# Optimization experiments

Hardware: AMD Instinct MI355X
Metric: run time of the kernel (lower is better)

The kernel has to match this reference:

```python
import jax, jax.numpy as jnp
import numpy as np

DIM_E, DIM_M, DIM_C = 1024, 64, 128
B, N = 4, 4096


def setup_inputs() -> dict:
    key = jax.random.key(0)
    ks = jax.random.split(key, 10)
    s = 1.0 / np.sqrt(DIM_E + DIM_C)
    return {
        "e": jax.random.normal(ks[0], (B, N, DIM_E), jnp.float32),
        "m": jax.random.normal(ks[1], (B, N, DIM_M), jnp.float32),
        "c": jax.random.normal(ks[2], (B, N, DIM_C), jnp.float32),
        "l": jax.random.uniform(ks[3], (B, N), jnp.float32),
        "Wq": jax.random.uniform(ks[4], (DIM_E + DIM_C, DIM_E), jnp.float32, -s, s),
        "bq": jax.random.uniform(ks[5], (DIM_E,), jnp.float32, -s, s),
        "Wk": jax.random.uniform(ks[6], (DIM_E + DIM_C, DIM_E), jnp.float32, -s, s),
        "bk": jax.random.uniform(ks[7], (DIM_E,), jnp.float32, -s, s),
        "Wv": jax.random.uniform(ks[8], (DIM_E + DIM_C, DIM_E), jnp.float32, -s, s),
        "bv": jax.random.uniform(ks[9], (DIM_E,), jnp.float32, -s, s),
    }


def reference(e, m, c, l, Wq, bq, Wk, bk, Wv, bv):
    x = jnp.concatenate([e, c], axis=-1)                       # [B,N,De+Dc]
    q = jnp.einsum('bnd,df->bnf', x, Wq) + bq                  # [B,N,De]
    k = jnp.einsum('bnd,df->bnf', x, Wk) + bk
    v = jnp.einsum('bnd,df->bnf', x, Wv) + bv
    scale = 1.0 / jnp.sqrt(jnp.asarray(q.shape[-1], q.dtype))
    attn_scores = jnp.einsum('bqd,bkd->bqk', q, k) * scale     # [B,N,N]
    membrane_mask = jnp.einsum('bqm,bkm->bqk', m, m)           # [B,N,N]
    lifespan_mask = l[:, :, None] * l[:, None, :]              # [B,N,N]
    adaptive_scores = attn_scores * membrane_mask * lifespan_mask
    attn_weights = jax.nn.softmax(adaptive_scores, axis=-1)
    h_tilde = jnp.einsum('bqk,bkd->bqd', attn_weights, v)      # [B,N,De]
    e_new = e + h_tilde
    return (e_new, h_tilde)
```

## Files before the change

### kernel.cpp

```cpp
#include <hip/hip_runtime.h>
#include <hip/hip_bf16.h>

#define DE 1024
#define DM 64
#define DC 128
#define DX 1152
#define NB 4
#define NN 4096
#define NT 16384

typedef _Float16 f16;
typedef _Float16 f16x4 __attribute__((ext_vector_type(4)));
typedef _Float16 f16x8 __attribute__((ext_vector_type(8)));
typedef float f32x4 __attribute__((ext_vector_type(4)));

__device__ __forceinline__ void g2l16(const void* g, void* l) {
  __builtin_amdgcn_global_load_lds(
      (const __attribute__((address_space(1))) unsigned int*)(unsigned long long)g,
      (__attribute__((address_space(3))) unsigned int*)(unsigned int)(unsigned long long)l,
      16, 0, 0);
}

__global__ void build_x_kernel(const float* __restrict__ e, const float* __restrict__ c,
                               f16* __restrict__ Xb) {
  const int total = NT * DX / 4;
  for (int i = blockIdx.x * blockDim.x + threadIdx.x; i < total; i += gridDim.x * blockDim.x) {
    int idx = i * 4;
    int r = idx / DX, col = idx - r * DX;
    float4 v;
    if (col < DE) v = *(const float4*)(e + (long)r * DE + col);
    else          v = *(const float4*)(c + (long)r * DC + (col - DE));
    f16x4 o = { (f16)v.x, (f16)v.y, (f16)v.z, (f16)v.w };
    *(f16x4*)(Xb + (long)idx) = o;
  }
}

__global__ void conv_f16_kernel(const float* __restrict__ in, f16* __restrict__ out, int total4) {
  for (int i = blockIdx.x * blockDim.x + threadIdx.x; i < total4; i += gridDim.x * blockDim.x) {
    float4 v = *(const float4*)(in + (long)i * 4);
    f16x4 o = { (f16)v.x, (f16)v.y, (f16)v.z, (f16)v.w };
    *(f16x4*)(out + (long)i * 4) = o;
  }
}

__global__ void transpose_w_kernel(const float* __restrict__ in, f16* __restrict__ out) {
  __shared__ float tile[32][33];
  int c0 = blockIdx.x * 32, r0 = blockIdx.y * 32;
  int x = threadIdx.x, y = threadIdx.y;
#pragma unroll
  for (int i = 0; i < 4; ++i)
    tile[y + 8 * i][x] = in[(long)(r0 + y + 8 * i) * DE + (c0 + x)];
  __syncthreads();
#pragma unroll
  for (int i = 0; i < 4; ++i)
    out[(long)(c0 + y + 8 * i) * DX + (r0 + x)] = (f16)tile[x][y + 8 * i];
}

__device__ __forceinline__ void mm_loop(const f16* __restrict__ A, const f16* __restrict__ B,
                                        int lda, int ldb, int K,
                                        f16* lA, f16* lB, f32x4 (&acc)[4][4]) {
  const int t = threadIdx.x;
  const int lane = t & 63;
  const int wid = t >> 6;
  const int wr = (wid >> 1) * 64, wc = (wid & 1) * 64;
  const int fr = lane & 15, fq = lane >> 4;
  for (int k0 = 0; k0 < K; k0 += 32) {
    __syncthreads();
#pragma unroll
    for (int it = 0; it < 2; ++it) {
      int byteoff = it * 4096 + t * 16;
      int row = byteoff >> 6;
      int ke = (byteoff & 63) >> 1;
      g2l16(A + (long)row * lda + k0 + ke, lA + (byteoff >> 1));
      g2l16(B + (long)row * ldb + k0 + ke, lB + (byteoff >> 1));
    }
    __syncthreads();
    f16x8 af[4], bfr[4];
#pragma unroll
    for (int i = 0; i < 4; ++i) {
      af[i]  = *(const f16x8*)(lA + (wr + i * 16 + fr) * 32 + fq * 8);
      bfr[i] = *(const f16x8*)(lB + (wc + i * 16 + fr) * 32 + fq * 8);
    }
#pragma unroll
    for (int m = 0; m < 4; ++m)
#pragma unroll
      for (int n = 0; n < 4; ++n)
        acc[m][n] = __builtin_amdgcn_mfma_f32_16x16x32_f16(af[m], bfr[n], acc[m][n], 0, 0, 0);
  }
}

__global__ __launch_bounds__(256) void mask_kernel(
    const f16* __restrict__ mb, const float* __restrict__ l, f16* __restrict__ Pm) {
  __shared__ __attribute__((aligned(16))) f16 lA[128 * 32], lB[128 * 32];
  f32x4 acc[4][4];
#pragma unroll
  for (int m = 0; m < 4; ++m)
#pragma unroll
    for (int n = 0; n < 4; ++n) acc[m][n] = (f32x4){0.f, 0.f, 0.f, 0.f};
  const int b = blockIdx.z;
  const int row0 = blockIdx.x * 128, col0 = blockIdx.y * 128;
  mm_loop(mb + (long)(b * NN + row0) * DM, mb + (long)(b * NN + col0) * DM,
          DM, DM, DM, lA, lB, acc);
  const int lane = threadIdx.x & 63, wid = threadIdx.x >> 6;
  const int wr = (wid >> 1) * 64, wc = (wid & 1) * 64;
  const int fr = lane & 15, fq = lane >> 4;
  const float* lb = l + (long)b * NN;
  f16* out = Pm + (long)b * NN * NN;
#pragma unroll
  for (int n = 0; n < 4; ++n) {
    int col = col0 + wc + n * 16 + fr;
    float lc = lb[col] * 0.03125f;
#pragma unroll
    for (int m = 0; m < 4; ++m)
#pragma unroll
      for (int r = 0; r < 4; ++r) {
        int row = row0 + wr + m * 16 + fq * 4 + r;
        out[(long)row * NN + col] = (f16)(acc[m][n][r] * lc * lb[row]);
      }
  }
}

__device__ __forceinline__ void gemm4_core(
    const f16* __restrict__ A, long lda,
    const f16* __restrict__ B, long ldb,
    int NTt, char* ldsb, f32x4 (&acc)[4][4]) {
  const int tid = threadIdx.x;
  const int lane = tid & 63, wid = tid >> 6;
  const int wr = wid >> 1, wc = wid & 1;
  const int fr = lane & 15, fq = lane >> 4;
  const int cb0 = ((fq) ^ (fr & 7)) << 4;
  const int cb1 = ((4 | fq) ^ (fr & 7)) << 4;

  auto stage = [&](const f16* __restrict__ S, long ld, int kt, char* base) {
#pragma unroll
    for (int it = 0; it < 4; ++it) {
      int off = it * 4096 + tid * 16;
      int sw = off ^ (((off >> 7) & 7) << 4);
      int row = sw >> 7;
      int colf = ((sw >> 4) & 7) << 3;
      g2l16(S + (long)row * ld + kt * 64 + colf, base + off);
    }
  };

  stage(A, lda, 0, ldsb);
  stage(B, ldb, 0, ldsb + 16384);
  __syncthreads();

  for (int tt = 0; tt < NTt; ++tt) {
    const int par = tt & 1;
    const char* cur = ldsb + par * 32768;
    char* nxt = ldsb + (par ^ 1) * 32768;
    if (tt + 1 < NTt) {
      stage(A, lda, tt + 1, nxt);
      stage(B, ldb, tt + 1, nxt + 16384);
    }
    __builtin_amdgcn_sched_barrier(0);
    f16x8 a[4][2], b[4][2];
#pragma unroll
    for (int i = 0; i < 4; ++i) {
      int row = wr * 64 + i * 16 + fr;
      a[i][0] = *(const f16x8*)(const void*)(cur + row * 128 + cb0);
      a[i][1] = *(const f16x8*)(const void*)(cur + row * 128 + cb1);
    }
#pragma unroll
    for (int i = 0; i < 4; ++i) {
      int row = wc * 64 + i * 16 + fr;
      b[i][0] = *(const f16x8*)(const void*)(cur + 16384 + row * 128 + cb0);
      b[i][1] = *(const f16x8*)(const void*)(cur + 16384 + row * 128 + cb1);
    }
    __builtin_amdgcn_s_setprio(1);
#pragma unroll
    for (int k = 0; k < 2; ++k)
#pragma unroll
      for (int m = 0; m < 4; ++m)
#pragma unroll
        for (int n = 0; n < 4; ++n)
          acc[m][n] = __builtin_amdgcn_mfma_f32_16x16x32_f16(a[m][k], b[n][k], acc[m][n], 0, 0, 0);
    __builtin_amdgcn_s_setprio(0);
    __syncthreads();
  }
}

__device__ __forceinline__ void swz_grid(int& bx, int& by, int& bz) {
  int nx = gridDim.x, ny = gridDim.y;
  int flat = blockIdx.x + nx * (blockIdx.y + ny * blockIdx.z);
  int total = nx * ny * gridDim.z;
  int cpx = total >> 3;
  flat = (flat & 7) * cpx + (flat >> 3);
  bx = flat % nx; int r = flat / nx;
  by = r % ny; bz = r / ny;
}

#define ACC_INIT()                                                  \
  f32x4 acc[4][4];                                                  \
  _Pragma("unroll") for (int m_ = 0; m_ < 4; ++m_)                  \
  _Pragma("unroll") for (int n_ = 0; n_ < 4; ++n_)                  \
      acc[m_][n_] = (f32x4){0.f, 0.f, 0.f, 0.f};

#define EPI4_IDX()                                                  \
  const int lane = threadIdx.x & 63, wid = threadIdx.x >> 6;        \
  const int wr = wid >> 1, wc = wid & 1;                            \
  const int fr = lane & 15, fq = lane >> 4;

__global__ __launch_bounds__(256, 2) void qk8_kernel(
    const f16* __restrict__ Xb, const f16* __restrict__ Wt,
    const float* __restrict__ bq, const float* __restrict__ bk,
    f16* __restrict__ qb, f16* __restrict__ kb) {
  __shared__ __attribute__((aligned(128))) char ldsb[65536];
  int bx, by, bz; swz_grid(bx, by, bz);
  const int row0 = bx * 128, col0 = by * 128;
  ACC_INIT();
  gemm4_core(Xb + (long)row0 * DX, DX, Wt + (long)col0 * DX, DX, DX / 64, ldsb, acc);
  EPI4_IDX();
  const bool isq = col0 < DE;
  const float* bvec = isq ? bq : bk;
  f16* ob = isq ? qb : kb;
  const int cbase = (isq ? col0 : col0 - DE) + wc * 64;
  const int rbase = row0 + wr * 64;
#pragma unroll
  for (int n = 0; n < 4; ++n) {
    int col = cbase + n * 16 + fr;
    float bb = bvec[col];
#pragma unroll
    for (int m = 0; m < 4; ++m)
#pragma unroll
      for (int j = 0; j < 4; ++j) {
        int row = rbase + m * 16 + fq * 4 + j;
        ob[(long)row * DE + col] = (f16)(acc[m][n][j] + bb);
      }
  }
}

__global__ __launch_bounds__(256, 2) void vt8_kernel(
    const f16* __restrict__ WtV, const f16* __restrict__ Xb,
    const float* __restrict__ bv, f16* __restrict__ Vt) {
  __shared__ __attribute__((aligned(128))) char ldsb[65536];
  int bx, by, bz; swz_grid(bx, by, bz);
  const int row0 = bx * 128, col0 = by * 128;
  ACC_INIT();
  gemm4_core(WtV + (long)row0 * DX, DX, Xb + (long)col0 * DX, DX, DX / 64, ldsb, acc);
  EPI4_IDX();
  const int cbase = col0 + wc * 64;
  const int rbase = row0 + wr * 64;
#pragma unroll
  for (int n = 0; n < 4; ++n) {
    int col = cbase + n * 16 + fr;
#pragma unroll
    for (int m = 0; m < 4; ++m)
#pragma unroll
      for (int j = 0; j < 4; ++j) {
        int row = rbase + m * 16 + fq * 4 + j;
        Vt[(long)row * NT + col] = (f16)(acc[m][n][j] + bv[row]);
      }
  }
}

__global__ __launch_bounds__(256, 2) void sc8_kernel(
    const f16* __restrict__ qb_, const f16* __restrict__ kb_, float* __restrict__ S) {
  __shared__ __attribute__((aligned(128))) char ldsb[65536];
  int bx, by, bz; swz_grid(bx, by, bz);
  const int row0 = bx * 128, col0 = by * 128;
  ACC_INIT();
  gemm4_core(qb_ + (long)row0 * DE, DE, kb_ + (long)col0 * DE, DE, DE / 64, ldsb, acc);
  EPI4_IDX();
  const int cbase = col0 + wc * 64;
  const int rbase = row0 + wr * 64;
#pragma unroll
  for (int n = 0; n < 4; ++n) {
    int col = cbase + n * 16 + fr;
#pragma unroll
    for (int m = 0; m < 4; ++m)
#pragma unroll
      for (int j = 0; j < 4; ++j) {
        int row = rbase + m * 16 + fq * 4 + j;
        S[(long)row * NN + col] = acc[m][n][j];
      }
  }
}

__global__ __launch_bounds__(256, 2) void pv8_kernel(
    const f16* __restrict__ P, const f16* __restrict__ Vt,
    const float* __restrict__ e, float* __restrict__ outE, float* __restrict__ outH) {
  __shared__ __attribute__((aligned(128))) char ldsb[65536];
  int bx, by, bz; swz_grid(bx, by, bz);
  const int b = bz;
  const int row0 = bx * 128, col0 = by * 128;
  ACC_INIT();
  gemm4_core(P + (long)b * NN * NN + (long)row0 * NN, NN,
             Vt + (long)col0 * NT + (long)b * NN, NT, NN / 64, ldsb, acc);
  EPI4_IDX();
  const int cbase = col0 + wc * 64;
  const int rbase = row0 + wr * 64;
#pragma unroll
  for (int n = 0; n < 4; ++n) {
    int col = cbase + n * 16 + fr;
#pragma unroll
    for (int m = 0; m < 4; ++m)
#pragma unroll
      for (int j = 0; j < 4; ++j) {
        int row = rbase + m * 16 + fq * 4 + j;
        long idx = ((long)b * NN + row) * DE + col;
        float h = acc[m][n][j];
        outE[idx] = e[idx] + h;
        outH[idx] = h;
      }
  }
}

__global__ __launch_bounds__(256) void softmax_kernel(const float* __restrict__ S,
                                                      const f16* __restrict__ Pm,
                                                      f16* __restrict__ P) {
  __shared__ float red[8];
  const long row = blockIdx.x;
  const float* s = S + row * NN;
  const f16* pmr = Pm + row * NN;
  const int t = threadIdx.x;
  float4 v[4];
  float mx = -3.0e38f;
#pragma unroll
  for (int i = 0; i < 4; ++i) {
    v[i] = *(const float4*)(s + t * 4 + i * 1024);
    f16x4 m4 = *(const f16x4*)(pmr + t * 4 + i * 1024);
    v[i].x *= (float)m4[0]; v[i].y *= (float)m4[1];
    v[i].z *= (float)m4[2]; v[i].w *= (float)m4[3];
    mx = fmaxf(mx, fmaxf(fmaxf(v[i].x, v[i].y), fmaxf(v[i].z, v[i].w)));
  }
#pragma unroll
  for (int o = 32; o; o >>= 1) mx = fmaxf(mx, __shfl_xor(mx, o));
  if ((t & 63) == 0) red[t >> 6] = mx;
  __syncthreads();
  mx = fmaxf(fmaxf(red[0], red[1]), fmaxf(red[2], red[3]));
  float sum = 0.f;
#pragma unroll
  for (int i = 0; i < 4; ++i) {
    v[i].x = __expf(v[i].x - mx); v[i].y = __expf(v[i].y - mx);
    v[i].z = __expf(v[i].z - mx); v[i].w = __expf(v[i].w - mx);
    sum += v[i].x + v[i].y + v[i].z + v[i].w;
  }
#pragma unroll
  for (int o = 32; o; o >>= 1) sum += __shfl_xor(sum, o);
  if ((t & 63) == 0) red[4 + (t >> 6)] = sum;
  __syncthreads();
  float inv = 1.f / (red[4] + red[5] + red[6] + red[7]);
  f16* p = P + row * NN;
#pragma unroll
  for (int i = 0; i < 4; ++i) {
    f16x4 o4 = { (f16)(v[i].x * inv), (f16)(v[i].y * inv),
                 (f16)(v[i].z * inv), (f16)(v[i].w * inv) };
    *(f16x4*)(p + t * 4 + i * 1024) = o4;
  }
}

extern "C" void kernel_launch(void* const* d_in, const int* in_sizes, int n_in,
                              void* d_out, int out_size, void* d_ws, size_t ws_size,
                              hipStream_t stream) {
  const float* e  = (const float*)d_in[0];
  const float* m  = (const float*)d_in[1];
  const float* c  = (const float*)d_in[2];
  const float* l  = (const float*)d_in[3];
  const float* Wq = (const float*)d_in[4];
  const float* bq = (const float*)d_in[5];
  const float* Wk = (const float*)d_in[6];
  const float* bk = (const float*)d_in[7];
  const float* Wv = (const float*)d_in[8];
  const float* bv = (const float*)d_in[9];
  float* outE = (float*)d_out;
  float* outH = outE + (long)NT * DE;

  char* ws = (char*)d_ws;
  size_t off = 0;
  auto alloc = [&](size_t bytes) {
    char* p = ws + off;
    off += (bytes + 255) & ~(size_t)255;
    return p;
  };
  f16* Xb    = (f16*)alloc((size_t)NT * DX * 2);
  f16* WtQK  = (f16*)alloc((size_t)2048 * DX * 2);
  f16* WtV   = (f16*)alloc((size_t)DE * DX * 2);
  f16* qb    = (f16*)alloc((size_t)NT * DE * 2);
  f16* kb    = (f16*)alloc((size_t)NT * DE * 2);
  f16* Vt    = (f16*)alloc((size_t)DE * NT * 2);
  f16* mb    = (f16*)alloc((size_t)NT * DM * 2);
  float* S   = (float*)alloc((size_t)NN * NN * 4);
  f16* P     = (f16*)alloc((size_t)NB * NN * NN * 2);
  if (off > ws_size) return;

  build_x_kernel<<<2048, 256, 0, stream>>>(e, c, Xb);
  conv_f16_kernel<<<512, 256, 0, stream>>>(m, mb, NT * DM / 4);
  transpose_w_kernel<<<dim3(32, 36), dim3(32, 8), 0, stream>>>(Wq, WtQK);
  transpose_w_kernel<<<dim3(32, 36), dim3(32, 8), 0, stream>>>(Wk, WtQK + (size_t)DE * DX);
  transpose_w_kernel<<<dim3(32, 36), dim3(32, 8), 0, stream>>>(Wv, WtV);
  mask_kernel<<<dim3(32, 32, NB), 256, 0, stream>>>(mb, l, P);
  qk8_kernel<<<dim3(128, 16), 256, 0, stream>>>(Xb, WtQK, bq, bk, qb, kb);
  vt8_kernel<<<dim3(8, 128), 256, 0, stream>>>(WtV, Xb, bv, Vt);
  for (int b = 0; b < NB; ++b) {
    sc8_kernel<<<dim3(32, 32), 256, 0, stream>>>(
        qb + (size_t)b * NN * DE, kb + (size_t)b * NN * DE, S);
    softmax_kernel<<<NN, 256, 0, stream>>>(S, P + (size_t)b * NN * NN, P + (size_t)b * NN * NN);
  }
  pv8_kernel<<<dim3(32, 8, NB), 256, 0, stream>>>(P, Vt, e, outE, outH);
}
```

Before: 739.5 us.

## Fuse membrane/lifespan mask into score GEMM and drop double-buffered LDS pipeline

Removes the standalone mask kernel and computes the m·mᵀ product with the lifespan scaling inside the score kernel epilogue, so softmax no longer reads a precomputed f16 mask. This eliminates writing and reading a B×N×N f16 mask tensor. Separately, the shared GEMM core switches from double-buffered LDS prefetching to a single buffer with load/sync per k-tile, halving LDS use and removing the min-blocks launch bound. That loses overlap of global loads with MFMA work in all GEMMs.

```diff
diff --git a/kernel.cpp b/kernel.cpp
--- a/kernel.cpp
+++ b/kernel.cpp
@@ -56,70 +56,6 @@
     out[(long)(c0 + y + 8 * i) * DX + (r0 + x)] = (f16)tile[x][y + 8 * i];
 }
 
-__device__ __forceinline__ void mm_loop(const f16* __restrict__ A, const f16* __restrict__ B,
-                                        int lda, int ldb, int K,
-                                        f16* lA, f16* lB, f32x4 (&acc)[4][4]) {
-  const int t = threadIdx.x;
-  const int lane = t & 63;
-  const int wid = t >> 6;
-  const int wr = (wid >> 1) * 64, wc = (wid & 1) * 64;
-  const int fr = lane & 15, fq = lane >> 4;
-  for (int k0 = 0; k0 < K; k0 += 32) {
-    __syncthreads();
-#pragma unroll
-    for (int it = 0; it < 2; ++it) {
-      int byteoff = it * 4096 + t * 16;
-      int row = byteoff >> 6;
-      int ke = (byteoff & 63) >> 1;
-      g2l16(A + (long)row * lda + k0 + ke, lA + (byteoff >> 1));
-      g2l16(B + (long)row * ldb + k0 + ke, lB + (byteoff >> 1));
-    }
-    __syncthreads();
-    f16x8 af[4], bfr[4];
-#pragma unroll
-    for (int i = 0; i < 4; ++i) {
-      af[i]  = *(const f16x8*)(lA + (wr + i * 16 + fr) * 32 + fq * 8);
-      bfr[i] = *(const f16x8*)(lB + (wc + i * 16 + fr) * 32 + fq * 8);
-    }
-#pragma unroll
-    for (int m = 0; m < 4; ++m)
-#pragma unroll
-      for (int n = 0; n < 4; ++n)
-        acc[m][n] = __builtin_amdgcn_mfma_f32_16x16x32_f16(af[m], bfr[n], acc[m][n], 0, 0, 0);
-  }
-}
-
-__global__ __launch_bounds__(256) void mask_kernel(
-    const f16* __restrict__ mb, const float* __restrict__ l, f16* __restrict__ Pm) {
-  __shared__ __attribute__((aligned(16))) f16 lA[128 * 32], lB[128 * 32];
-  f32x4 acc[4][4];
-#pragma unroll
-  for (int m = 0; m < 4; ++m)
-#pragma unroll
-    for (int n = 0; n < 4; ++n) acc[m][n] = (f32x4){0.f, 0.f, 0.f, 0.f};
-  const int b = blockIdx.z;
-  const int row0 = blockIdx.x * 128, col0 = blockIdx.y * 128;
-  mm_loop(mb + (long)(b * NN + row0) * DM, mb + (long)(b * NN + col0) * DM,
-          DM, DM, DM, lA, lB, acc);
-  const int lane = threadIdx.x & 63, wid = threadIdx.x >> 6;
-  const int wr = (wid >> 1) * 64, wc = (wid & 1) * 64;
-  const int fr = lane & 15, fq = lane >> 4;
-  const float* lb = l + (long)b * NN;
-  f16* out = Pm + (long)b * NN * NN;
-#pragma unroll
-  for (int n = 0; n < 4; ++n) {
-    int col = col0 + wc + n * 16 + fr;
-    float lc = lb[col] * 0.03125f;
-#pragma unroll
-    for (int m = 0; m < 4; ++m)
-#pragma unroll
-      for (int r = 0; r < 4; ++r) {
-        int row = row0 + wr + m * 16 + fq * 4 + r;
-        out[(long)row * NN + col] = (f16)(acc[m][n][r] * lc * lb[row]);
-      }
-  }
-}
-
 __device__ __forceinline__ void gemm4_core(
     const f16* __restrict__ A, long lda,
     const f16* __restrict__ B, long ldb,
@@ -142,31 +78,23 @@
     }
   };
 
-  stage(A, lda, 0, ldsb);
-  stage(B, ldb, 0, ldsb + 16384);
-  __syncthreads();
-
   for (int tt = 0; tt < NTt; ++tt) {
-    const int par = tt & 1;
-    const char* cur = ldsb + par * 32768;
-    char* nxt = ldsb + (par ^ 1) * 32768;
-    if (tt + 1 < NTt) {
-      stage(A, lda, tt + 1, nxt);
-      stage(B, ldb, tt + 1, nxt + 16384);
-    }
-    __builtin_amdgcn_sched_barrier(0);
+    __syncthreads();
+    stage(A, lda, tt, ldsb);
+    stage(B, ldb, tt, ldsb + 16384);
+    __syncthreads();
     f16x8 a[4][2], b[4][2];
 #pragma unroll
     for (int i = 0; i < 4; ++i) {
       int row = wr * 64 + i * 16 + fr;
-      a[i][0] = *(const f16x8*)(const void*)(cur + row * 128 + cb0);
-      a[i][1] = *(const f16x8*)(const void*)(cur + row * 128 + cb1);
+      a[i][0] = *(const f16x8*)(const void*)(ldsb + row * 128 + cb0);
+      a[i][1] = *(const f16x8*)(const void*)(ldsb + row * 128 + cb1);
     }
 #pragma unroll
     for (int i = 0; i < 4; ++i) {
       int row = wc * 64 + i * 16 + fr;
-      b[i][0] = *(const f16x8*)(const void*)(cur + 16384 + row * 128 + cb0);
-      b[i][1] = *(const f16x8*)(const void*)(cur + 16384 + row * 128 + cb1);
+      b[i][0] = *(const f16x8*)(const void*)(ldsb + 16384 + row * 128 + cb0);
+      b[i][1] = *(const f16x8*)(const void*)(ldsb + 16384 + row * 128 + cb1);
     }
     __builtin_amdgcn_s_setprio(1);
 #pragma unroll
@@ -177,7 +105,6 @@
         for (int n = 0; n < 4; ++n)
           acc[m][n] = __builtin_amdgcn_mfma_f32_16x16x32_f16(a[m][k], b[n][k], acc[m][n], 0, 0, 0);
     __builtin_amdgcn_s_setprio(0);
-    __syncthreads();
   }
 }
 
@@ -191,25 +118,25 @@
   by = r % ny; bz = r / ny;
 }
 
-#define ACC_INIT()                                                  \
-  f32x4 acc[4][4];                                                  \
+#define ACC_INIT(nm)                                                \
+  f32x4 nm[4][4];                                                   \
   _Pragma("unroll") for (int m_ = 0; m_ < 4; ++m_)                  \
   _Pragma("unroll") for (int n_ = 0; n_ < 4; ++n_)                  \
-      acc[m_][n_] = (f32x4){0.f, 0.f, 0.f, 0.f};
+      nm[m_][n_] = (f32x4){0.f, 0.f, 0.f, 0.f};
 
 #define EPI4_IDX()                                                  \
   const int lane = threadIdx.x & 63, wid = threadIdx.x >> 6;        \
   const int wr = wid >> 1, wc = wid & 1;                            \
   const int fr = lane & 15, fq = lane >> 4;
 
-__global__ __launch_bounds__(256, 2) void qk8_kernel(
+__global__ __launch_bounds__(256) void qk8_kernel(
     const f16* __restrict__ Xb, const f16* __restrict__ Wt,
     const float* __restrict__ bq, const float* __restrict__ bk,
     f16* __restrict__ qb, f16* __restrict__ kb) {
-  __shared__ __attribute__((aligned(128))) char ldsb[65536];
+  __shared__ __attribute__((aligned(128))) char ldsb[32768];
   int bx, by, bz; swz_grid(bx, by, bz);
   const int row0 = bx * 128, col0 = by * 128;
-  ACC_INIT();
+  ACC_INIT(acc);
   gemm4_core(Xb + (long)row0 * DX, DX, Wt + (long)col0 * DX, DX, DX / 64, ldsb, acc);
   EPI4_IDX();
   const bool isq = col0 < DE;
@@ -231,13 +158,13 @@
   }
 }
 
-__global__ __launch_bounds__(256, 2) void vt8_kernel(
+__global__ __launch_bounds__(256) void vt8_kernel(
     const f16* __restrict__ WtV, const f16* __restrict__ Xb,
     const float* __restrict__ bv, f16* __restrict__ Vt) {
-  __shared__ __attribute__((aligned(128))) char ldsb[65536];
+  __shared__ __attribute__((aligned(128))) char ldsb[32768];
   int bx, by, bz; swz_grid(bx, by, bz);
   const int row0 = bx * 128, col0 = by * 128;
-  ACC_INIT();
+  ACC_INIT(acc);
   gemm4_core(WtV + (long)row0 * DX, DX, Xb + (long)col0 * DX, DX, DX / 64, ldsb, acc);
   EPI4_IDX();
   const int cbase = col0 + wc * 64;
@@ -255,37 +182,43 @@
   }
 }
 
-__global__ __launch_bounds__(256, 2) void sc8_kernel(
-    const f16* __restrict__ qb_, const f16* __restrict__ kb_, float* __restrict__ S) {
-  __shared__ __attribute__((aligned(128))) char ldsb[65536];
+__global__ __launch_bounds__(256) void sc8_kernel(
+    const f16* __restrict__ qb_, const f16* __restrict__ kb_,
+    const f16* __restrict__ mb_, const float* __restrict__ l_,
+    float* __restrict__ S) {
+  __shared__ __attribute__((aligned(128))) char ldsb[32768];
   int bx, by, bz; swz_grid(bx, by, bz);
   const int row0 = bx * 128, col0 = by * 128;
-  ACC_INIT();
+  ACC_INIT(acc);
   gemm4_core(qb_ + (long)row0 * DE, DE, kb_ + (long)col0 * DE, DE, DE / 64, ldsb, acc);
+  ACC_INIT(am);
+  gemm4_core(mb_ + (long)row0 * DM, DM, mb_ + (long)col0 * DM, DM, 1, ldsb, am);
   EPI4_IDX();
   const int cbase = col0 + wc * 64;
   const int rbase = row0 + wr * 64;
+  const float scale = 0.03125f;
 #pragma unroll
   for (int n = 0; n < 4; ++n) {
     int col = cbase + n * 16 + fr;
+    float lc = l_[col] * scale;
 #pragma unroll
     for (int m = 0; m < 4; ++m)
 #pragma unroll
       for (int j = 0; j < 4; ++j) {
         int row = rbase + m * 16 + fq * 4 + j;
-        S[(long)row * NN + col] = acc[m][n][j];
+        S[(long)row * NN + col] = acc[m][n][j] * am[m][n][j] * lc * l_[row];
       }
   }
 }
 
-__global__ __launch_bounds__(256, 2) void pv8_kernel(
+__global__ __launch_bounds__(256) void pv8_kernel(
     const f16* __restrict__ P, const f16* __restrict__ Vt,
     const float* __restrict__ e, float* __restrict__ outE, float* __restrict__ outH) {
-  __shared__ __attribute__((aligned(128))) char ldsb[65536];
+  __shared__ __attribute__((aligned(128))) char ldsb[32768];
   int bx, by, bz; swz_grid(bx, by, bz);
   const int b = bz;
   const int row0 = bx * 128, col0 = by * 128;
-  ACC_INIT();
+  ACC_INIT(acc);
   gemm4_core(P + (long)b * NN * NN + (long)row0 * NN, NN,
              Vt + (long)col0 * NT + (long)b * NN, NT, NN / 64, ldsb, acc);
   EPI4_IDX();
@@ -308,21 +241,16 @@
 }
 
 __global__ __launch_bounds__(256) void softmax_kernel(const float* __restrict__ S,
-                                                      const f16* __restrict__ Pm,
                                                       f16* __restrict__ P) {
   __shared__ float red[8];
   const long row = blockIdx.x;
   const float* s = S + row * NN;
-  const f16* pmr = Pm + row * NN;
   const int t = threadIdx.x;
   float4 v[4];
   float mx = -3.0e38f;
 #pragma unroll
   for (int i = 0; i < 4; ++i) {
     v[i] = *(const float4*)(s + t * 4 + i * 1024);
-    f16x4 m4 = *(const f16x4*)(pmr + t * 4 + i * 1024);
-    v[i].x *= (float)m4[0]; v[i].y *= (float)m4[1];
-    v[i].z *= (float)m4[2]; v[i].w *= (float)m4[3];
     mx = fmaxf(mx, fmaxf(fmaxf(v[i].x, v[i].y), fmaxf(v[i].z, v[i].w)));
   }
 #pragma unroll
@@ -390,13 +318,13 @@
   transpose_w_kernel<<<dim3(32, 36), dim3(32, 8), 0, stream>>>(Wq, WtQK);
   transpose_w_kernel<<<dim3(32, 36), dim3(32, 8), 0, stream>>>(Wk, WtQK + (size_t)DE * DX);
   transpose_w_kernel<<<dim3(32, 36), dim3(32, 8), 0, stream>>>(Wv, WtV);
-  mask_kernel<<<dim3(32, 32, NB), 256, 0, stream>>>(mb, l, P);
   qk8_kernel<<<dim3(128, 16), 256, 0, stream>>>(Xb, WtQK, bq, bk, qb, kb);
   vt8_kernel<<<dim3(8, 128), 256, 0, stream>>>(WtV, Xb, bv, Vt);
   for (int b = 0; b < NB; ++b) {
     sc8_kernel<<<dim3(32, 32), 256, 0, stream>>>(
-        qb + (size_t)b * NN * DE, kb + (size_t)b * NN * DE, S);
-    softmax_kernel<<<NN, 256, 0, stream>>>(S, P + (size_t)b * NN * NN, P + (size_t)b * NN * NN);
+        qb + (size_t)b * NN * DE, kb + (size_t)b * NN * DE,
+        mb + (size_t)b * NN * DM, l + (size_t)b * NN, S);
+    softmax_kernel<<<NN, 256, 0, stream>>>(S, P + (size_t)b * NN * NN);
   }
   pv8_kernel<<<dim3(32, 8, NB), 256, 0, stream>>>(P, Vt, e, outE, outH);
 }
```

Measured after the change: 777.1 us. +5.1%, slower.
